# Kernel optimization log

Measured on AMD Instinct MI355X. Metric: run time of the kernel, lower is better.

Reference implementation:

```python
import jax, jax.numpy as jnp
import numpy as np

NUM_ACTIVE = 2  # top-k active experts

def setup_inputs() -> dict:
    key = jax.random.key(0)
    ks = jax.random.split(key, 5)
    B, N, D, H, E = 8192, 16, 128, 384, 8
    x = jax.random.normal(ks[0], (B, N, D), dtype=jnp.float32)
    # xavier-ish scales for stability
    router_w = jax.random.normal(ks[1], (E, N * D), dtype=jnp.float32) * (1.0 / np.sqrt(N * D))
    w1 = jax.random.normal(ks[2], (E, N, D, H), dtype=jnp.float32) * (1.0 / np.sqrt(D))
    w_gate = jax.random.normal(ks[3], (E, N, D, H), dtype=jnp.float32) * (1.0 / np.sqrt(D))
    w2 = jax.random.normal(ks[4], (E, N, H, D), dtype=jnp.float32) * (1.0 / np.sqrt(H))
    return {"x": x, "router_w": router_w, "w1": w1, "w_gate": w_gate, "w2": w2}

def reference(x, router_w, w1, w_gate, w2):
    B, N, D = x.shape
    E = w1.shape[0]
    # shared router over flattened heads
    router_logits = x.reshape(B, N * D) @ router_w.T            # (B, E)
    topk_logits, topk_idx = jax.lax.top_k(router_logits, NUM_ACTIVE)
    topk_w = jax.nn.softmax(topk_logits, axis=-1)               # (B, K)
    # combined routing weight per (token, expert); zero if expert not selected
    onehot = jax.nn.one_hot(topk_idx, E, dtype=x.dtype)         # (B, K, E)
    w_tok_exp = jnp.einsum('bk,bke->be', topk_w, onehot)        # (B, E)
    out = jnp.zeros_like(x)
    # loop over fixed, small expert count; unselected tokens get weight 0
    for e in range(E):
        h1 = jnp.einsum('bnd,ndh->bnh', x, w1[e])
        gate = jnp.einsum('bnd,ndh->bnh', x, w_gate[e])
        h = h1 * jax.nn.silu(gate)                              # SwiGLU (dropout=0 / eval)
        out_e = jnp.einsum('bnh,nhd->bnd', h, w2[e])
        out = out + w_tok_exp[:, e][:, None, None] * out_e
    return out
```

## Files before the change

kernel.cpp:

```cpp
#include <hip/hip_runtime.h>

#define NTOK  8192
#define NHEAD 16
#define DDIM  128
#define HDIM  384
#define NEXP  8
#define TILE  128
#define PADN  9216
#define ENTRIES 1280

typedef __attribute__((ext_vector_type(8))) short short8;
typedef __attribute__((ext_vector_type(4))) float f32x4;

#define SZ_WP    (128UL*12*24*512*2)
#define OFF_WP   0UL
#define OFF_ROUT (OFF_WP + SZ_WP)
#define OFF_CNT  (OFF_ROUT + 8192UL*16)
#define OFF_TAB  (OFF_CNT + 256)
#define OFF_LIST (OFF_TAB + 2UL*ENTRIES*16)
#define OFF_POS  (OFF_LIST + 2UL*PADN*4)
#define OFF_WL   (OFF_POS + 2UL*NTOK*4)
#define OFF_XG   (OFF_WL + 2UL*PADN*4)
#define XG_SLOT  (16UL*PADN*128*2)

struct Routing { int i0, i1; float w0, w1; };

__device__ __forceinline__ unsigned short f2bf(float f) {
  unsigned int u = __float_as_uint(f);
  u += 0x7fffu + ((u >> 16) & 1u);
  return (unsigned short)(u >> 16);
}

__device__ __forceinline__ void dma16(const unsigned short* g, char* l) {
  __builtin_amdgcn_global_load_lds(
      (const __attribute__((address_space(1))) unsigned int*)g,
      (__attribute__((address_space(3))) unsigned int*)l, 16, 0, 0);
}

__global__ __launch_bounds__(256) void convA_kernel(
    const float* __restrict__ w1, const float* __restrict__ wg,
    unsigned short* __restrict__ wP) {
  __shared__ float ls[32][388];
  const int kk = blockIdx.x;
  const int en = blockIdx.y;
  const int z  = blockIdx.z;
  const float* src = (z == 0 ? w1 : wg) + ((size_t)en * DDIM + kk * 32) * HDIM;
  const int tid = threadIdx.x;
  #pragma unroll
  for (int i = 0; i < 12; ++i) {
    int f4 = i * 256 + tid;
    int row = f4 / 96, c4 = f4 % 96;
    float4 v = reinterpret_cast<const float4*>(src + (size_t)row * HDIM)[c4];
    ls[row][c4*4+0] = v.x; ls[row][c4*4+1] = v.y;
    ls[row][c4*4+2] = v.z; ls[row][c4*4+3] = v.w;
  }
  __syncthreads();
  #pragma unroll
  for (int i = 0; i < 6; ++i) {
    int fid = i * 256 + tid;
    int ct = fid >> 6, lane = fid & 63;
    int r0 = (lane >> 4) * 8, c = ct * 16 + (lane & 15);
    unsigned short o[8];
    #pragma unroll
    for (int j = 0; j < 8; ++j) o[j] = f2bf(ls[r0 + j][c]);
    size_t off = (((size_t)en * 12 + (ct >> 1)) * 24 + (z * 8 + kk * 2 + (ct & 1))) * 512
               + (size_t)lane * 8;
    reinterpret_cast<uint4*>(wP + off)[0] =
        make_uint4((unsigned)o[0] | ((unsigned)o[1] << 16),
                   (unsigned)o[2] | ((unsigned)o[3] << 16),
                   (unsigned)o[4] | ((unsigned)o[5] << 16),
                   (unsigned)o[6] | ((unsigned)o[7] << 16));
  }
}

__global__ __launch_bounds__(256) void convB_kernel(
    const float* __restrict__ w2, unsigned short* __restrict__ wP) {
  __shared__ float ls[32][132];
  const int kk = blockIdx.x;
  const int en = blockIdx.y;
  const float* src = w2 + ((size_t)en * HDIM + kk * 32) * DDIM;
  const int tid = threadIdx.x;
  #pragma unroll
  for (int i = 0; i < 4; ++i) {
    int f4 = i * 256 + tid;
    int row = f4 >> 5, c4 = f4 & 31;
    float4 v = reinterpret_cast<const float4*>(src + (size_t)row * DDIM)[c4];
    ls[row][c4*4+0] = v.x; ls[row][c4*4+1] = v.y;
    ls[row][c4*4+2] = v.z; ls[row][c4*4+3] = v.w;
  }
  __syncthreads();
  #pragma unroll
  for (int i = 0; i < 2; ++i) {
    int fid = i * 256 + tid;
    int ct = fid >> 6, lane = fid & 63;
    int r0 = (lane >> 4) * 8, c = ct * 16 + (lane & 15);
    unsigned short o[8];
    #pragma unroll
    for (int j = 0; j < 8; ++j) o[j] = f2bf(ls[r0 + j][c]);
    size_t off = (((size_t)en * 12 + kk) * 24 + (16 + ct)) * 512 + (size_t)lane * 8;
    reinterpret_cast<uint4*>(wP + off)[0] =
        make_uint4((unsigned)o[0] | ((unsigned)o[1] << 16),
                   (unsigned)o[2] | ((unsigned)o[3] << 16),
                   (unsigned)o[4] | ((unsigned)o[5] << 16),
                   (unsigned)o[6] | ((unsigned)o[7] << 16));
  }
}

__global__ __launch_bounds__(256) void router_kernel(
    const float* __restrict__ x, const float* __restrict__ rw,
    Routing* __restrict__ routing) {
  const int lane = threadIdx.x & 63;
  const int wgid = blockIdx.x * 4 + (threadIdx.x >> 6);
  const int tok0 = wgid * 4;
  float acc[4][8];
  #pragma unroll
  for (int t = 0; t < 4; ++t)
    #pragma unroll
    for (int e = 0; e < 8; ++e) acc[t][e] = 0.f;
  const float4* xr = reinterpret_cast<const float4*>(x);
  const float4* wr = reinterpret_cast<const float4*>(rw);
  #pragma unroll
  for (int c = 0; c < 8; ++c) {
    float4 wv[8];
    #pragma unroll
    for (int e = 0; e < 8; ++e) wv[e] = wr[e * 512 + c * 64 + lane];
    #pragma unroll
    for (int t = 0; t < 4; ++t) {
      float4 xv = xr[(size_t)(tok0 + t) * 512 + c * 64 + lane];
      #pragma unroll
      for (int e = 0; e < 8; ++e)
        acc[t][e] += xv.x * wv[e].x + xv.y * wv[e].y + xv.z * wv[e].z + xv.w * wv[e].w;
    }
  }
  #pragma unroll
  for (int t = 0; t < 4; ++t)
    #pragma unroll
    for (int e = 0; e < 8; ++e) {
      acc[t][e] += __shfl_xor(acc[t][e], 1);
      acc[t][e] += __shfl_xor(acc[t][e], 2);
      acc[t][e] += __shfl_xor(acc[t][e], 4);
    }
  const int l3 = lane & 7;
  #pragma unroll
  for (int t = 0; t < 4; ++t) {
    float v0 = (l3 & 1) ? acc[t][1] : acc[t][0];
    float v1 = (l3 & 1) ? acc[t][3] : acc[t][2];
    float v2 = (l3 & 1) ? acc[t][5] : acc[t][4];
    float v3 = (l3 & 1) ? acc[t][7] : acc[t][6];
    float u0 = (l3 & 2) ? v1 : v0;
    float u1 = (l3 & 2) ? v3 : v2;
    float sel = (l3 & 4) ? u1 : u0;
    sel += __shfl_xor(sel, 8);
    sel += __shfl_xor(sel, 16);
    sel += __shfl_xor(sel, 32);
    float le[8];
    #pragma unroll
    for (int e = 0; e < 8; ++e) le[e] = __shfl(sel, e);
    if (lane == 0) {
      int tok = tok0 + t;
      int i0 = 0; float m0 = le[0];
      #pragma unroll
      for (int e = 1; e < 8; ++e) if (le[e] > m0) { m0 = le[e]; i0 = e; }
      int i1 = -1; float m1 = -3.4e38f;
      #pragma unroll
      for (int e = 0; e < 8; ++e) if (e != i0 && le[e] > m1) { m1 = le[e]; i1 = e; }
      float ed = __expf(m1 - m0);
      Routing r; r.i0 = i0; r.i1 = i1;
      r.w0 = 1.f / (1.f + ed); r.w1 = ed / (1.f + ed);
      routing[tok] = r;
    }
  }
}

__global__ __launch_bounds__(256) void count_kernel(
    const Routing* __restrict__ routing, int* __restrict__ cnt) {
  const int s = blockIdx.x >> 3, e = blockIdx.x & 7;
  const int tid = threadIdx.x;
  int c = 0;
  for (int t = tid; t < NTOK; t += 256) {
    Routing r = routing[t];
    c += ((s == 0 ? r.i0 : r.i1) == e);
  }
  c += __shfl_xor(c, 32); c += __shfl_xor(c, 16); c += __shfl_xor(c, 8);
  c += __shfl_xor(c, 4);  c += __shfl_xor(c, 2);  c += __shfl_xor(c, 1);
  __shared__ int wsum[4];
  if ((tid & 63) == 0) wsum[tid >> 6] = c;
  __syncthreads();
  if (tid == 0) cnt[blockIdx.x] = wsum[0] + wsum[1] + wsum[2] + wsum[3];
}

__global__ void build_kernel(const int* __restrict__ cnt, int* __restrict__ cur,
                             int4* __restrict__ table, int* __restrict__ list) {
  const int tid = threadIdx.x;
  for (int i = tid; i < 2 * ENTRIES; i += 256)
    table[i] = make_int4(0, 0, 0, 0);
  for (int i = tid; i < 2 * PADN; i += 256)
    list[i] = -1;
  __syncthreads();
  if (tid < 16) {
    int s = tid >> 3, e = tid & 7;
    int b = 0;
    for (int k = 0; k < e; ++k) b += ((cnt[s * 8 + k] + 127) >> 7) << 7;
    cur[tid] = b;
  }
  __syncthreads();
  if (tid < 16) {
    int s = tid >> 3, xcd = tid & 7;
    int j = 0, ab = 0;
    for (int e = 0; e < 8; ++e) {
      int c = cnt[s * 8 + e];
      #pragma unroll
      for (int nn = 0; nn < 2; ++nn) {
        int n = xcd + nn * 8;
        for (int t = 0; t < c; t += TILE) {
          int rc = c - t; if (rc > TILE) rc = TILE;
          table[s * ENTRIES + xcd + 8 * j] = make_int4(e, ab + t, rc, n);
          ++j;
        }
      }
      ab += ((c + 127) >> 7) << 7;
    }
  }
}

__global__ __launch_bounds__(256) void compact_kernel(
    const Routing* __restrict__ routing, const int* __restrict__ cur,
    int* __restrict__ list, float* __restrict__ wl, int* __restrict__ posmap) {
  const int s = blockIdx.x >> 3, e = blockIdx.x & 7;
  const int tid = threadIdx.x;
  __shared__ int ps[256];
  int myc = 0;
  for (int t = tid; t < NTOK; t += 256) {
    Routing r = routing[t];
    myc += ((s == 0 ? r.i0 : r.i1) == e);
  }
  ps[tid] = myc;
  __syncthreads();
  for (int off = 1; off < 256; off <<= 1) {
    int v = (tid >= off) ? ps[tid - off] : 0;
    __syncthreads();
    ps[tid] += v;
    __syncthreads();
  }
  int base = cur[blockIdx.x] + ps[tid] - myc;
  for (int t = tid; t < NTOK; t += 256) {
    Routing r = routing[t];
    int ei = (s == 0 ? r.i0 : r.i1);
    if (ei == e) {
      list[s * PADN + base] = t;
      wl[s * PADN + base] = (s == 0 ? r.w0 : r.w1);
      posmap[s * NTOK + t] = base;
      ++base;
    }
  }
}

__global__ __launch_bounds__(256) void gather_kernel(
    const float* __restrict__ x, const int* __restrict__ posmap,
    unsigned short* __restrict__ xg0, unsigned short* __restrict__ xg1,
    const int mode) {
  const int tid = threadIdx.x;
  const int n = tid >> 4, j = tid & 15;
  for (int it = 0; it < 32; ++it) {
    int t = blockIdx.x * 32 + it;
    const float* src = x + ((size_t)t * NHEAD + n) * DDIM + j * 8;
    float4 v0 = reinterpret_cast<const float4*>(src)[0];
    float4 v1 = reinterpret_cast<const float4*>(src)[1];
    uint4 w = make_uint4(
        (unsigned)f2bf(v0.x) | ((unsigned)f2bf(v0.y) << 16),
        (unsigned)f2bf(v0.z) | ((unsigned)f2bf(v0.w) << 16),
        (unsigned)f2bf(v1.x) | ((unsigned)f2bf(v1.y) << 16),
        (unsigned)f2bf(v1.z) | ((unsigned)f2bf(v1.w) << 16));
    if (mode != 2) {
      int p0 = posmap[t];
      *reinterpret_cast<uint4*>(xg0 + ((size_t)n * PADN + p0) * 128 + ((j ^ (p0 & 7)) * 8)) = w;
    }
    if (mode != 1) {
      int p1 = posmap[NTOK + t];
      *reinterpret_cast<uint4*>(xg1 + ((size_t)n * PADN + p1) * 128 + ((j ^ (p1 & 7)) * 8)) = w;
    }
  }
}

__global__ __launch_bounds__(512, 2) void expert_kernel(
    const unsigned short* __restrict__ xg,
    const unsigned short* __restrict__ wP,
    const int* __restrict__ list, const float* __restrict__ wl,
    const int4* __restrict__ table,
    float* __restrict__ out, const int slot)
{
  extern __shared__ char smem[];
  char* wb  = smem;
  char* pwb = smem + 49152;
  const int4 tb = table[slot * ENTRIES + blockIdx.x];
  const int e = tb.x, rbeg = tb.y, rcnt = tb.z, n = tb.w;
  if (rcnt == 0) return;
  const int* lst = list + slot * PADN + rbeg;
  const float* wls = wl + slot * PADN + rbeg;
  const int tid = threadIdx.x;
  const int wid = tid >> 6, lane = tid & 63;
  const int lr = lane & 15, lq = lane >> 4;
  const int tq = wid >> 1, ch = wid & 1;
  char* pq = pwb + tq * 2304;
  const f32x4 z4 = {0.f, 0.f, 0.f, 0.f};

  const unsigned short* wsrc = wP + (size_t)(e * NHEAD + n) * (12 * 24 * 512);
  const unsigned short* xpan = xg + ((size_t)n * PADN + rbeg) * 128;

  #pragma unroll
  for (int i = 0; i < 4; ++i)
    dma16(xpan + (size_t)wid * 2048 + i * 512 + lane * 8, wb + wid * 4096 + i * 1024);
  asm volatile("s_waitcnt vmcnt(0)" ::: "memory");
  __builtin_amdgcn_s_barrier();

  short8 a[2][4];
  #pragma unroll
  for (int mi = 0; mi < 2; ++mi) {
    int row = tq * 32 + mi * 16 + lr;
    #pragma unroll
    for (int kk = 0; kk < 4; ++kk)
      a[mi][kk] = *reinterpret_cast<const short8*>(
          wb + row * 256 + ((kk * 64 + lq * 16) ^ ((row & 7) << 4)));
  }
  asm volatile("s_waitcnt lgkmcnt(0)" ::: "memory");
  __builtin_amdgcn_sched_barrier(0);
  __builtin_amdgcn_s_barrier();

  f32x4 acc[2][4];
  #pragma unroll
  for (int mi = 0; mi < 2; ++mi)
    #pragma unroll
    for (int ct = 0; ct < 4; ++ct) acc[mi][ct] = z4;

  #pragma unroll
  for (int i = 0; i < 3; ++i) {
    int seg = wid * 3 + i;
    dma16(wsrc + (size_t)seg * 512 + lane * 8, wb + seg * 1024);
  }

  #pragma unroll
  for (int c = 0; c < 12; ++c) {
    const int p = c & 1;
    char* wbp = wb + p * 24576;

    asm volatile("s_waitcnt lgkmcnt(0)" ::: "memory");
    __builtin_amdgcn_s_barrier();
    __builtin_amdgcn_sched_barrier(0);

    if (c < 11) {
      char* wbn = wb + (p ^ 1) * 24576;
      #pragma unroll
      for (int i = 0; i < 3; ++i) {
        int seg = wid * 3 + i;
        dma16(wsrc + ((size_t)(c + 1) * 24 + seg) * 512 + lane * 8, wbn + seg * 1024);
      }
      asm volatile("s_waitcnt vmcnt(3)" ::: "memory");
    } else {
      asm volatile("s_waitcnt vmcnt(0)" ::: "memory");
    }
    __builtin_amdgcn_s_barrier();
    __builtin_amdgcn_sched_barrier(0);

    {
      f32x4 ah[2], ag[2];
      ah[0] = ah[1] = z4; ag[0] = ag[1] = z4;
      #pragma unroll
      for (int kk = 0; kk < 4; ++kk) {
        short8 b1 = *reinterpret_cast<const short8*>(wbp + (kk * 2 + ch) * 1024 + lane * 16);
        short8 bg = *reinterpret_cast<const short8*>(wbp + 8192 + (kk * 2 + ch) * 1024 + lane * 16);
        #pragma unroll
        for (int mi = 0; mi < 2; ++mi) {
          ah[mi] = __builtin_amdgcn_mfma_f32_16x16x32_bf16(a[mi][kk], b1, ah[mi], 0, 0, 0);
          ag[mi] = __builtin_amdgcn_mfma_f32_16x16x32_bf16(a[mi][kk], bg, ag[mi], 0, 0, 0);
        }
      }
      #pragma unroll
      for (int mi = 0; mi < 2; ++mi)
        #pragma unroll
        for (int r = 0; r < 4; ++r) {
          float h1 = ah[mi][r], g = ag[mi][r];
          float val = h1 * g * __builtin_amdgcn_rcpf(1.f + __expf(-g));
          int rowq = mi * 16 + lq * 4 + r;
          int h = ch * 16 + lr;
          *reinterpret_cast<unsigned short*>(pq + rowq * 72 + h * 2) = f2bf(val);
        }
    }

    asm volatile("s_waitcnt lgkmcnt(0)" ::: "memory");
    __builtin_amdgcn_s_barrier();
    __builtin_amdgcn_sched_barrier(0);

    {
      short8 a2[2];
      #pragma unroll
      for (int mi = 0; mi < 2; ++mi)
        a2[mi] = *reinterpret_cast<const short8*>(pq + (mi * 16 + lr) * 72 + lq * 16);
      #pragma unroll
      for (int ct = 0; ct < 4; ++ct) {
        short8 b = *reinterpret_cast<const short8*>(wbp + (16 + ch * 4 + ct) * 1024 + lane * 16);
        acc[0][ct] = __builtin_amdgcn_mfma_f32_16x16x32_bf16(a2[0], b, acc[0][ct], 0, 0, 0);
        acc[1][ct] = __builtin_amdgcn_mfma_f32_16x16x32_bf16(a2[1], b, acc[1][ct], 0, 0, 0);
      }
    }
  }

  #pragma unroll
  for (int mi = 0; mi < 2; ++mi)
    #pragma unroll
    for (int r = 0; r < 4; ++r) {
      int row = tq * 32 + mi * 16 + lq * 4 + r;
      if (row < rcnt) {
        int tok = lst[row];
        float wt = wls[row];
        float* op = out + ((size_t)tok * NHEAD + n) * DDIM;
        #pragma unroll
        for (int ct = 0; ct < 4; ++ct) {
          int col = (ch * 4 + ct) * 16 + lr;
          float v = acc[mi][ct][r] * wt;
          if (slot == 0) op[col] = v;
          else          op[col] += v;
        }
      }
    }
}

extern "C" void kernel_launch(void* const* d_in, const int* in_sizes, int n_in,
                              void* d_out, int out_size, void* d_ws, size_t ws_size,
                              hipStream_t stream) {
  const float* x  = (const float*)d_in[0];
  const float* rw = (const float*)d_in[1];
  const float* w1 = (const float*)d_in[2];
  const float* wg = (const float*)d_in[3];
  const float* w2 = (const float*)d_in[4];
  float* out = (float*)d_out;
  char* ws = (char*)d_ws;

  unsigned short* wP = (unsigned short*)(ws + OFF_WP);
  Routing* routing = (Routing*)(ws + OFF_ROUT);
  int* cnt = (int*)(ws + OFF_CNT);
  int* cur = cnt + 16;
  int4* table = (int4*)(ws + OFF_TAB);
  int* list = (int*)(ws + OFF_LIST);
  int* posmap = (int*)(ws + OFF_POS);
  float* wl = (float*)(ws + OFF_WL);
  unsigned short* xg0 = (unsigned short*)(ws + OFF_XG);

  const bool dual = (ws_size >= OFF_XG + 2 * XG_SLOT);
  unsigned short* xg1 = dual ? (unsigned short*)(ws + OFF_XG + XG_SLOT) : xg0;

  convA_kernel<<<dim3(4, 128, 2), 256, 0, stream>>>(w1, wg, wP);
  convB_kernel<<<dim3(12, 128, 1), 256, 0, stream>>>(w2, wP);
  router_kernel<<<512, 256, 0, stream>>>(x, rw, routing);
  count_kernel<<<16, 256, 0, stream>>>(routing, cnt);
  build_kernel<<<1, 256, 0, stream>>>(cnt, cur, table, list);
  compact_kernel<<<16, 256, 0, stream>>>(routing, cur, list, wl, posmap);

  if (dual) {
    gather_kernel<<<256, 256, 0, stream>>>(x, posmap, xg0, xg1, 0);
    expert_kernel<<<ENTRIES, 512, 58368, stream>>>(xg0, wP, list, wl, table, out, 0);
    expert_kernel<<<ENTRIES, 512, 58368, stream>>>(xg1, wP, list, wl, table, out, 1);
  } else {
    gather_kernel<<<256, 256, 0, stream>>>(x, posmap, xg0, xg0, 1);
    expert_kernel<<<ENTRIES, 512, 58368, stream>>>(xg0, wP, list, wl, table, out, 0);
    gather_kernel<<<256, 256, 0, stream>>>(x, posmap, xg0, xg0, 2);
    expert_kernel<<<ENTRIES, 512, 58368, stream>>>(xg0, wP, list, wl, table, out, 1);
  }
}
```

Before: 296.7 us.

## Keep expert weight half resident in LDS and loop token tiles per block

The expert kernel no longer streams the full weight panel per 128-token tile. Each block now loads half of one (expert, head) weight set (144 KB) into LDS once and loops over every token tile of that expert. The H dimension is split into two halves run as separate launches that accumulate into the output. The table build step is removed, and x tiles are read straight from global memory without the swizzle. This cuts repeated weight traffic, but it drops occupancy to one block per CU, removes the load/compute double buffering, and leaves only 256 blocks, so per-expert token imbalance can cause tail effects.

```diff
diff --git a/kernel.cpp b/kernel.cpp
--- a/kernel.cpp
+++ b/kernel.cpp
@@ -5,9 +5,7 @@
 #define DDIM  128
 #define HDIM  384
 #define NEXP  8
-#define TILE  128
 #define PADN  9216
-#define ENTRIES 1280
 
 typedef __attribute__((ext_vector_type(8))) short short8;
 typedef __attribute__((ext_vector_type(4))) float f32x4;
@@ -16,8 +14,7 @@
 #define OFF_WP   0UL
 #define OFF_ROUT (OFF_WP + SZ_WP)
 #define OFF_CNT  (OFF_ROUT + 8192UL*16)
-#define OFF_TAB  (OFF_CNT + 256)
-#define OFF_LIST (OFF_TAB + 2UL*ENTRIES*16)
+#define OFF_LIST (OFF_CNT + 256)
 #define OFF_POS  (OFF_LIST + 2UL*PADN*4)
 #define OFF_WL   (OFF_POS + 2UL*NTOK*4)
 #define OFF_XG   (OFF_WL + 2UL*PADN*4)
@@ -189,37 +186,13 @@
   if (tid == 0) cnt[blockIdx.x] = wsum[0] + wsum[1] + wsum[2] + wsum[3];
 }
 
-__global__ void build_kernel(const int* __restrict__ cnt, int* __restrict__ cur,
-                             int4* __restrict__ table, int* __restrict__ list) {
-  const int tid = threadIdx.x;
-  for (int i = tid; i < 2 * ENTRIES; i += 256)
-    table[i] = make_int4(0, 0, 0, 0);
-  for (int i = tid; i < 2 * PADN; i += 256)
-    list[i] = -1;
-  __syncthreads();
+__global__ void build_kernel(const int* __restrict__ cnt, int* __restrict__ cur) {
+  int tid = threadIdx.x;
   if (tid < 16) {
     int s = tid >> 3, e = tid & 7;
     int b = 0;
     for (int k = 0; k < e; ++k) b += ((cnt[s * 8 + k] + 127) >> 7) << 7;
     cur[tid] = b;
-  }
-  __syncthreads();
-  if (tid < 16) {
-    int s = tid >> 3, xcd = tid & 7;
-    int j = 0, ab = 0;
-    for (int e = 0; e < 8; ++e) {
-      int c = cnt[s * 8 + e];
-      #pragma unroll
-      for (int nn = 0; nn < 2; ++nn) {
-        int n = xcd + nn * 8;
-        for (int t = 0; t < c; t += TILE) {
-          int rc = c - t; if (rc > TILE) rc = TILE;
-          table[s * ENTRIES + xcd + 8 * j] = make_int4(e, ab + t, rc, n);
-          ++j;
-        }
-      }
-      ab += ((c + 127) >> 7) << 7;
-    }
   }
 }
 
@@ -273,30 +246,30 @@
         (unsigned)f2bf(v1.z) | ((unsigned)f2bf(v1.w) << 16));
     if (mode != 2) {
       int p0 = posmap[t];
-      *reinterpret_cast<uint4*>(xg0 + ((size_t)n * PADN + p0) * 128 + ((j ^ (p0 & 7)) * 8)) = w;
+      *reinterpret_cast<uint4*>(xg0 + ((size_t)n * PADN + p0) * 128 + j * 8) = w;
     }
     if (mode != 1) {
       int p1 = posmap[NTOK + t];
-      *reinterpret_cast<uint4*>(xg1 + ((size_t)n * PADN + p1) * 128 + ((j ^ (p1 & 7)) * 8)) = w;
-    }
-  }
-}
-
-__global__ __launch_bounds__(512, 2) void expert_kernel(
+      *reinterpret_cast<uint4*>(xg1 + ((size_t)n * PADN + p1) * 128 + j * 8) = w;
+    }
+  }
+}
+
+__global__ __launch_bounds__(512, 1) void expert_kernel(
     const unsigned short* __restrict__ xg,
     const unsigned short* __restrict__ wP,
     const int* __restrict__ list, const float* __restrict__ wl,
-    const int4* __restrict__ table,
-    float* __restrict__ out, const int slot)
+    const int* __restrict__ cnt,
+    float* __restrict__ out, const int slot, const int h, const int mode)
 {
   extern __shared__ char smem[];
-  char* wb  = smem;
-  char* pwb = smem + 49152;
-  const int4 tb = table[slot * ENTRIES + blockIdx.x];
-  const int e = tb.x, rbeg = tb.y, rcnt = tb.z, n = tb.w;
-  if (rcnt == 0) return;
-  const int* lst = list + slot * PADN + rbeg;
-  const float* wls = wl + slot * PADN + rbeg;
+  char* pwb = smem + 147456;
+  const int bid = blockIdx.x;
+  const int e = bid >> 5, n = (bid >> 1) & 15, tp = bid & 1;
+  const int cntE  = cnt[slot * 8 + e];
+  const int ebase = cnt[16 + slot * 8 + e];
+  const int ntiles = (cntE + 127) >> 7;
+  if (cntE == 0) return;
   const int tid = threadIdx.x;
   const int wid = tid >> 6, lane = tid & 63;
   const int lr = lane & 15, lq = lane >> 4;
@@ -304,124 +277,101 @@
   char* pq = pwb + tq * 2304;
   const f32x4 z4 = {0.f, 0.f, 0.f, 0.f};
 
-  const unsigned short* wsrc = wP + (size_t)(e * NHEAD + n) * (12 * 24 * 512);
-  const unsigned short* xpan = xg + ((size_t)n * PADN + rbeg) * 128;
-
-  #pragma unroll
-  for (int i = 0; i < 4; ++i)
-    dma16(xpan + (size_t)wid * 2048 + i * 512 + lane * 8, wb + wid * 4096 + i * 1024);
+  const unsigned short* wsrc = wP + (size_t)(e * NHEAD + n) * (12 * 24 * 512)
+                                  + (size_t)h * 144 * 512;
+  #pragma unroll
+  for (int i = 0; i < 18; ++i) {
+    int seg = wid * 18 + i;
+    dma16(wsrc + (size_t)seg * 512 + lane * 8, smem + seg * 1024);
+  }
   asm volatile("s_waitcnt vmcnt(0)" ::: "memory");
-  __builtin_amdgcn_s_barrier();
-
-  short8 a[2][4];
-  #pragma unroll
-  for (int mi = 0; mi < 2; ++mi) {
-    int row = tq * 32 + mi * 16 + lr;
-    #pragma unroll
-    for (int kk = 0; kk < 4; ++kk)
-      a[mi][kk] = *reinterpret_cast<const short8*>(
-          wb + row * 256 + ((kk * 64 + lq * 16) ^ ((row & 7) << 4)));
-  }
-  asm volatile("s_waitcnt lgkmcnt(0)" ::: "memory");
-  __builtin_amdgcn_sched_barrier(0);
-  __builtin_amdgcn_s_barrier();
-
-  f32x4 acc[2][4];
-  #pragma unroll
-  for (int mi = 0; mi < 2; ++mi)
-    #pragma unroll
-    for (int ct = 0; ct < 4; ++ct) acc[mi][ct] = z4;
-
-  #pragma unroll
-  for (int i = 0; i < 3; ++i) {
-    int seg = wid * 3 + i;
-    dma16(wsrc + (size_t)seg * 512 + lane * 8, wb + seg * 1024);
-  }
-
-  #pragma unroll
-  for (int c = 0; c < 12; ++c) {
-    const int p = c & 1;
-    char* wbp = wb + p * 24576;
-
-    asm volatile("s_waitcnt lgkmcnt(0)" ::: "memory");
-    __builtin_amdgcn_s_barrier();
-    __builtin_amdgcn_sched_barrier(0);
-
-    if (c < 11) {
-      char* wbn = wb + (p ^ 1) * 24576;
-      #pragma unroll
-      for (int i = 0; i < 3; ++i) {
-        int seg = wid * 3 + i;
-        dma16(wsrc + ((size_t)(c + 1) * 24 + seg) * 512 + lane * 8, wbn + seg * 1024);
+  __syncthreads();
+
+  const unsigned short* xpan = xg + (size_t)n * PADN * 128;
+
+  for (int t = tp; t < ntiles; t += 2) {
+    const int pbase = ebase + t * 128;
+
+    short8 a[2][4];
+    #pragma unroll
+    for (int mi = 0; mi < 2; ++mi) {
+      int pos = pbase + tq * 32 + mi * 16 + lr;
+      #pragma unroll
+      for (int kk = 0; kk < 4; ++kk)
+        a[mi][kk] = *reinterpret_cast<const short8*>(
+            xpan + (size_t)pos * 128 + kk * 32 + lq * 8);
+    }
+
+    f32x4 acc[2][4];
+    #pragma unroll
+    for (int mi = 0; mi < 2; ++mi)
+      #pragma unroll
+      for (int ct = 0; ct < 4; ++ct) acc[mi][ct] = z4;
+
+    #pragma unroll
+    for (int c = 0; c < 6; ++c) {
+      char* wbp = smem + c * 24576;
+
+      {
+        f32x4 ah[2], ag[2];
+        ah[0] = ah[1] = z4; ag[0] = ag[1] = z4;
+        #pragma unroll
+        for (int kk = 0; kk < 4; ++kk) {
+          short8 b1 = *reinterpret_cast<const short8*>(wbp + (kk * 2 + ch) * 1024 + lane * 16);
+          short8 bg = *reinterpret_cast<const short8*>(wbp + 8192 + (kk * 2 + ch) * 1024 + lane * 16);
+          #pragma unroll
+          for (int mi = 0; mi < 2; ++mi) {
+            ah[mi] = __builtin_amdgcn_mfma_f32_16x16x32_bf16(a[mi][kk], b1, ah[mi], 0, 0, 0);
+            ag[mi] = __builtin_amdgcn_mfma_f32_16x16x32_bf16(a[mi][kk], bg, ag[mi], 0, 0, 0);
+          }
+        }
+        #pragma unroll
+        for (int mi = 0; mi < 2; ++mi)
+          #pragma unroll
+          for (int r = 0; r < 4; ++r) {
+            float h1 = ah[mi][r], g = ag[mi][r];
+            float val = h1 * g * __builtin_amdgcn_rcpf(1.f + __expf(-g));
+            int rowq = mi * 16 + lq * 4 + r;
+            int hh = ch * 16 + lr;
+            *reinterpret_cast<unsigned short*>(pq + rowq * 72 + hh * 2) = f2bf(val);
+          }
       }
-      asm volatile("s_waitcnt vmcnt(3)" ::: "memory");
-    } else {
-      asm volatile("s_waitcnt vmcnt(0)" ::: "memory");
-    }
-    __builtin_amdgcn_s_barrier();
-    __builtin_amdgcn_sched_barrier(0);
-
-    {
-      f32x4 ah[2], ag[2];
-      ah[0] = ah[1] = z4; ag[0] = ag[1] = z4;
-      #pragma unroll
-      for (int kk = 0; kk < 4; ++kk) {
-        short8 b1 = *reinterpret_cast<const short8*>(wbp + (kk * 2 + ch) * 1024 + lane * 16);
-        short8 bg = *reinterpret_cast<const short8*>(wbp + 8192 + (kk * 2 + ch) * 1024 + lane * 16);
+      __syncthreads();
+
+      {
+        short8 a2[2];
         #pragma unroll
-        for (int mi = 0; mi < 2; ++mi) {
-          ah[mi] = __builtin_amdgcn_mfma_f32_16x16x32_bf16(a[mi][kk], b1, ah[mi], 0, 0, 0);
-          ag[mi] = __builtin_amdgcn_mfma_f32_16x16x32_bf16(a[mi][kk], bg, ag[mi], 0, 0, 0);
+        for (int mi = 0; mi < 2; ++mi)
+          a2[mi] = *reinterpret_cast<const short8*>(pq + (mi * 16 + lr) * 72 + lq * 16);
+        #pragma unroll
+        for (int ct = 0; ct < 4; ++ct) {
+          short8 b = *reinterpret_cast<const short8*>(wbp + (16 + ch * 4 + ct) * 1024 + lane * 16);
+          acc[0][ct] = __builtin_amdgcn_mfma_f32_16x16x32_bf16(a2[0], b, acc[0][ct], 0, 0, 0);
+          acc[1][ct] = __builtin_amdgcn_mfma_f32_16x16x32_bf16(a2[1], b, acc[1][ct], 0, 0, 0);
         }
       }
-      #pragma unroll
-      for (int mi = 0; mi < 2; ++mi)
-        #pragma unroll
-        for (int r = 0; r < 4; ++r) {
-          float h1 = ah[mi][r], g = ag[mi][r];
-          float val = h1 * g * __builtin_amdgcn_rcpf(1.f + __expf(-g));
-          int rowq = mi * 16 + lq * 4 + r;
-          int h = ch * 16 + lr;
-          *reinterpret_cast<unsigned short*>(pq + rowq * 72 + h * 2) = f2bf(val);
-        }
-    }
-
-    asm volatile("s_waitcnt lgkmcnt(0)" ::: "memory");
-    __builtin_amdgcn_s_barrier();
-    __builtin_amdgcn_sched_barrier(0);
-
-    {
-      short8 a2[2];
-      #pragma unroll
-      for (int mi = 0; mi < 2; ++mi)
-        a2[mi] = *reinterpret_cast<const short8*>(pq + (mi * 16 + lr) * 72 + lq * 16);
-      #pragma unroll
-      for (int ct = 0; ct < 4; ++ct) {
-        short8 b = *reinterpret_cast<const short8*>(wbp + (16 + ch * 4 + ct) * 1024 + lane * 16);
-        acc[0][ct] = __builtin_amdgcn_mfma_f32_16x16x32_bf16(a2[0], b, acc[0][ct], 0, 0, 0);
-        acc[1][ct] = __builtin_amdgcn_mfma_f32_16x16x32_bf16(a2[1], b, acc[1][ct], 0, 0, 0);
-      }
-    }
-  }
-
-  #pragma unroll
-  for (int mi = 0; mi < 2; ++mi)
-    #pragma unroll
-    for (int r = 0; r < 4; ++r) {
-      int row = tq * 32 + mi * 16 + lq * 4 + r;
-      if (row < rcnt) {
-        int tok = lst[row];
-        float wt = wls[row];
-        float* op = out + ((size_t)tok * NHEAD + n) * DDIM;
-        #pragma unroll
-        for (int ct = 0; ct < 4; ++ct) {
-          int col = (ch * 4 + ct) * 16 + lr;
-          float v = acc[mi][ct][r] * wt;
-          if (slot == 0) op[col] = v;
-          else          op[col] += v;
+      __syncthreads();
+    }
+
+    #pragma unroll
+    for (int mi = 0; mi < 2; ++mi)
+      #pragma unroll
+      for (int r = 0; r < 4; ++r) {
+        int grow = t * 128 + tq * 32 + mi * 16 + lq * 4 + r;
+        if (grow < cntE) {
+          int tok = list[slot * PADN + ebase + grow];
+          float wt = wl[slot * PADN + ebase + grow];
+          float* op = out + ((size_t)tok * NHEAD + n) * DDIM;
+          #pragma unroll
+          for (int ct = 0; ct < 4; ++ct) {
+            int col = (ch * 4 + ct) * 16 + lr;
+            float v = acc[mi][ct][r] * wt;
+            if (mode == 0) op[col] = v;
+            else           op[col] += v;
+          }
         }
       }
-    }
+  }
 }
 
 extern "C" void kernel_launch(void* const* d_in, const int* in_sizes, int n_in,
@@ -439,7 +389,6 @@
   Routing* routing = (Routing*)(ws + OFF_ROUT);
   int* cnt = (int*)(ws + OFF_CNT);
   int* cur = cnt + 16;
-  int4* table = (int4*)(ws + OFF_TAB);
   int* list = (int*)(ws + OFF_LIST);
   int* posmap = (int*)(ws + OFF_POS);
   float* wl = (float*)(ws + OFF_WL);
@@ -452,17 +401,21 @@
   convB_kernel<<<dim3(12, 128, 1), 256, 0, stream>>>(w2, wP);
   router_kernel<<<512, 256, 0, stream>>>(x, rw, routing);
   count_kernel<<<16, 256, 0, stream>>>(routing, cnt);
-  build_kernel<<<1, 256, 0, stream>>>(cnt, cur, table, list);
+  build_kernel<<<1, 64, 0, stream>>>(cnt, cur);
   compact_kernel<<<16, 256, 0, stream>>>(routing, cur, list, wl, posmap);
 
   if (dual) {
     gather_kernel<<<256, 256, 0, stream>>>(x, posmap, xg0, xg1, 0);
-    expert_kernel<<<ENTRIES, 512, 58368, stream>>>(xg0, wP, list, wl, table, out, 0);
-    expert_kernel<<<ENTRIES, 512, 58368, stream>>>(xg1, wP, list, wl, table, out, 1);
+    expert_kernel<<<256, 512, 156672, stream>>>(xg0, wP, list, wl, cnt, out, 0, 0, 0);
+    expert_kernel<<<256, 512, 156672, stream>>>(xg0, wP, list, wl, cnt, out, 0, 1, 1);
+    expert_kernel<<<256, 512, 156672, stream>>>(xg1, wP, list, wl, cnt, out, 1, 0, 1);
+    expert_kernel<<<256, 512, 156672, stream>>>(xg1, wP, list, wl, cnt, out, 1, 1, 1);
   } else {
     gather_kernel<<<256, 256, 0, stream>>>(x, posmap, xg0, xg0, 1);
-    expert_kernel<<<ENTRIES, 512, 58368, stream>>>(xg0, wP, list, wl, table, out, 0);
+    expert_kernel<<<256, 512, 156672, stream>>>(xg0, wP, list, wl, cnt, out, 0, 0, 0);
+    expert_kernel<<<256, 512, 156672, stream>>>(xg0, wP, list, wl, cnt, out, 0, 1, 1);
     gather_kernel<<<256, 256, 0, stream>>>(x, posmap, xg0, xg0, 2);
-    expert_kernel<<<ENTRIES, 512, 58368, stream>>>(xg0, wP, list, wl, table, out, 1);
-  }
-}
+    expert_kernel<<<256, 512, 156672, stream>>>(xg0, wP, list, wl, cnt, out, 1, 0, 1);
+    expert_kernel<<<256, 512, 156672, stream>>>(xg0, wP, list, wl, cnt, out, 1, 1, 1);
+  }
+}
```

New measurement: 496.0 us. 1.67x slower.
